# Kernel tuning notes

Measured on AMD Instinct MI355X. Metric: run time of the kernel, lower is better.

Reference implementation:

```python
import jax, jax.numpy as jnp
import numpy as np

NUM_HEADS = 16
NUM_KV_HEADS = 4
HEAD_DIM = 64
HIDDEN = 1024
B, S = 2, 2048


def setup_inputs() -> dict:
    key = jax.random.key(0)
    ks = jax.random.split(key, 9)
    sc = 0.02
    return {
        "x": jax.random.normal(ks[0], (B, S, HIDDEN), dtype=jnp.float32),
        "Wq": jax.random.normal(ks[1], (HIDDEN, NUM_HEADS * HEAD_DIM), dtype=jnp.float32) * sc,
        "bq": jnp.zeros((NUM_HEADS * HEAD_DIM,), dtype=jnp.float32),
        "Wk": jax.random.normal(ks[2], (HIDDEN, NUM_KV_HEADS * HEAD_DIM), dtype=jnp.float32) * sc,
        "bk": jnp.zeros((NUM_KV_HEADS * HEAD_DIM,), dtype=jnp.float32),
        "Wv": jax.random.normal(ks[3], (HIDDEN, NUM_KV_HEADS * HEAD_DIM), dtype=jnp.float32) * sc,
        "bv": jnp.zeros((NUM_KV_HEADS * HEAD_DIM,), dtype=jnp.float32),
        "Wo": jax.random.normal(ks[4], (NUM_HEADS * HEAD_DIM, HIDDEN), dtype=jnp.float32) * sc,
        "bo": jnp.zeros((HIDDEN,), dtype=jnp.float32),
    }


def reference(x, Wq, bq, Wk, bk, Wv, bv, Wo, bo):
    bs, seq, _ = x.shape
    groups = NUM_HEADS // NUM_KV_HEADS
    # projections -> [B, H, S, D]
    q = (x @ Wq + bq).reshape(bs, seq, NUM_HEADS, HEAD_DIM).transpose(0, 2, 1, 3)
    k = (x @ Wk + bk).reshape(bs, seq, NUM_KV_HEADS, HEAD_DIM).transpose(0, 2, 1, 3)
    v = (x @ Wv + bv).reshape(bs, seq, NUM_KV_HEADS, HEAD_DIM).transpose(0, 2, 1, 3)
    # repeat_interleave KV heads to match query heads (GQA expansion)
    k = jnp.repeat(k, groups, axis=1)
    v = jnp.repeat(v, groups, axis=1)
    # NOTE: source applies NO 1/sqrt(d) scaling and no mask/ALiBi
    scores = jnp.einsum("bhqd,bhkd->bhqk", q, k)
    attn = jax.nn.softmax(scores.astype(jnp.float32), axis=-1).astype(q.dtype)
    out = jnp.einsum("bhqk,bhkd->bhqd", attn, v)
    out = out.transpose(0, 2, 1, 3).reshape(bs, seq, NUM_HEADS * HEAD_DIM)
    return out @ Wo + bo
```

## Files before the change

### kernel.cpp

```cpp
#include <hip/hip_runtime.h>

#define NHEADS 16
#define NKV    4
#define HDIM   64
#define HIDDEN 1024
#define BATCH  2
#define SEQ    2048
#define MROWS  (BATCH * SEQ)
#define LOG2E  1.44269504088896340736f

typedef __bf16 bf16_t;
typedef bf16_t bf16x8 __attribute__((ext_vector_type(8)));
typedef float  f32x4  __attribute__((ext_vector_type(4)));

__device__ __forceinline__ float bf2f(unsigned short u) {
    return __uint_as_float(((unsigned int)u) << 16);
}
__device__ __forceinline__ unsigned short f2bf(float f) {
    unsigned int u = __float_as_uint(f);
    u += 0x7FFFu + ((u >> 16) & 1u);
    return (unsigned short)(u >> 16);
}

__device__ __forceinline__ void gld16(const unsigned short* g, unsigned short* l)
{
    __builtin_amdgcn_global_load_lds(
        (const __attribute__((address_space(1))) void*)g,
        (__attribute__((address_space(3))) void*)l,
        16, 0, 0);
}

__device__ __forceinline__ int swz(int row, int ch) {
    return (row * 8 + (ch ^ (row & 7))) * 8;
}
__device__ __forceinline__ int swz16(int row, int ch) {
    return (row * 16 + (ch ^ (row & 7))) * 8;
}

__device__ __forceinline__ bool sniff_is_f32(const unsigned short* __restrict__ x)
{
    const int e = (x[threadIdx.x & 63] >> 7) & 0xFF;
    const unsigned long long ok = __ballot(e >= 110 && e <= 140);
    return __popcll(ok) < 56;
}

__device__ __forceinline__ void load8cvt(const void* base, size_t elem, bool isf32, unsigned short out[8])
{
    if (!isf32) {
        *(uint4*)out = *(const uint4*)((const unsigned short*)base + elem);
    } else {
        const float* p = (const float*)base + elem;
        float4 v0 = *(const float4*)p;
        float4 v1 = *(const float4*)(p + 4);
        out[0] = f2bf(v0.x); out[1] = f2bf(v0.y); out[2] = f2bf(v0.z); out[3] = f2bf(v0.w);
        out[4] = f2bf(v1.x); out[5] = f2bf(v1.y); out[6] = f2bf(v1.z); out[7] = f2bf(v1.w);
    }
}
__device__ __forceinline__ float bias_at(const void* b, int i, bool isf32)
{
    return isf32 ? ((const float*)b)[i] : bf2f(((const unsigned short*)b)[i]);
}

__global__ __launch_bounds__(256)
void prep_kernel(const void* __restrict__ x,
                 const void* __restrict__ Wq, const void* __restrict__ Wk,
                 const void* __restrict__ Wv, const void* __restrict__ Wo,
                 unsigned short* __restrict__ xb,
                 unsigned short* __restrict__ Wqkvt,
                 unsigned short* __restrict__ Wot)
{
    const bool isf32 = sniff_is_f32((const unsigned short*)x);
    const int t = threadIdx.x;
    int bid = blockIdx.x;

    if (bid < 2048) {
        if (!isf32) return;
        const size_t c = (size_t)bid * 256 + t;
        unsigned short v[8];
        load8cvt(x, c * 8, true, v);
        *(uint4*)(&xb[c * 8]) = *(uint4*)v;
        return;
    }
    bid -= 2048;
    const void* src; unsigned short* dst; int N, rowoff;
    if (bid < 256)      {             src = Wq; dst = Wqkvt; N = 1024; rowoff = 0;    }
    else if (bid < 320) { bid -= 256; src = Wk; dst = Wqkvt; N = 256;  rowoff = 1024; }
    else if (bid < 384) { bid -= 320; src = Wv; dst = Wqkvt; N = 256;  rowoff = 1280; }
    else                { bid -= 384; src = Wo; dst = Wot;   N = 1024; rowoff = 0;    }
    const int ntx = N / 64;
    const int gn0 = (bid % ntx) * 64;
    const int gk0 = (bid / ntx) * 64;

    __shared__ unsigned short Ts[64][72];
#pragma unroll
    for (int half = 0; half < 2; ++half) {
        const int kl = (t >> 3) + half * 32;
        const int n8 = (t & 7) * 8;
        unsigned short v[8];
        load8cvt(src, (size_t)(gk0 + kl) * N + gn0 + n8, isf32, v);
        *(uint4*)(&Ts[kl][n8]) = *(uint4*)v;
    }
    __syncthreads();
#pragma unroll
    for (int half = 0; half < 2; ++half) {
        const int nl = (t >> 3) + half * 32;
        const int k8 = (t & 7) * 8;
        unsigned short v[8];
#pragma unroll
        for (int j = 0; j < 8; ++j) v[j] = Ts[k8 + j][nl];
        *(uint4*)(&dst[(size_t)(rowoff + gn0 + nl) * HIDDEN + gk0 + k8]) = *(uint4*)v;
    }
}

template<int TBM, int TBN>
__device__ __forceinline__ void gemm_tile(const unsigned short* __restrict__ A,
                                          const unsigned short* __restrict__ Bt,
                                          int K, int m0, int n0,
                                          unsigned short* As, unsigned short* Bs,
                                          f32x4 (&acc)[TBM / 32][TBN / 32])
{
    const int tid  = threadIdx.x;
    const int lane = tid & 63;
    const int wave = tid >> 6;
    const int quad = lane >> 4;
    const int l15  = lane & 15;
    const int wr   = wave >> 1;
    const int wc   = wave & 1;

    for (int k0 = 0; k0 < K; k0 += 128) {
#pragma unroll
        for (int r = 0; r < TBM / 16; ++r) {
            const int u = r * 256 + tid;
            const int row = u >> 4;
            const int gch = ((u & 15) ^ (row & 7)) * 8;
            gld16(&A[(size_t)(m0 + row) * K + k0 + gch], &As[(r * 256 + wave * 64) * 8]);
        }
#pragma unroll
        for (int r = 0; r < TBN / 16; ++r) {
            const int u = r * 256 + tid;
            const int row = u >> 4;
            const int gch = ((u & 15) ^ (row & 7)) * 8;
            gld16(&Bt[(size_t)(n0 + row) * K + k0 + gch], &Bs[(r * 256 + wave * 64) * 8]);
        }
        __syncthreads();

#pragma unroll
        for (int kk = 0; kk < 4; ++kk) {
            bf16x8 af[TBM / 32], bfv[TBN / 32];
#pragma unroll
            for (int i = 0; i < TBM / 32; ++i)
                af[i] = *(const bf16x8*)(&As[swz16(wr * (TBM / 2) + i * 16 + l15, kk * 4 + quad)]);
#pragma unroll
            for (int j = 0; j < TBN / 32; ++j)
                bfv[j] = *(const bf16x8*)(&Bs[swz16(wc * (TBN / 2) + j * 16 + l15, kk * 4 + quad)]);
#pragma unroll
            for (int i = 0; i < TBM / 32; ++i)
#pragma unroll
                for (int j = 0; j < TBN / 32; ++j)
                    acc[i][j] = __builtin_amdgcn_mfma_f32_16x16x32_bf16(af[i], bfv[j], acc[i][j], 0, 0, 0);
        }
        __syncthreads();
    }
}

__global__ __launch_bounds__(256)
void gemm_qkv(const void* __restrict__ xraw,
              const unsigned short* __restrict__ xb,
              const unsigned short* __restrict__ Bt,
              const void* __restrict__ bq, const void* __restrict__ bk,
              const void* __restrict__ bv,
              unsigned short* __restrict__ Qh,
              unsigned short* __restrict__ Kh,
              unsigned short* __restrict__ Vt)
{
    __shared__ __align__(16) unsigned short As[128 * 128];
    __shared__ __align__(16) unsigned short Bs[64 * 128];
    const bool bias_f32 = sniff_is_f32((const unsigned short*)xraw);
    const unsigned short* A = bias_f32 ? xb : (const unsigned short*)xraw;
    const int lane = threadIdx.x & 63;
    const int wave = threadIdx.x >> 6;
    const int quad = lane >> 4, l15 = lane & 15;
    const int wr = wave >> 1, wc = wave & 1;
    const int m0 = blockIdx.y * 128, n0 = blockIdx.x * 64;

    f32x4 acc[4][2] = {};
    gemm_tile<128, 64>(A, Bt, HIDDEN, m0, n0, As, Bs, acc);

#pragma unroll
    for (int i = 0; i < 4; ++i) {
#pragma unroll
        for (int j = 0; j < 2; ++j) {
            const int nn  = n0 + wc * 32 + j * 16 + l15;
            const int mmb = m0 + wr * 64 + i * 16 + quad * 4;
            const int b = mmb >> 11, s0 = mmb & 2047;
            if (nn < 1024) {
                const float bias = bias_at(bq, nn, bias_f32);
                const int h = nn >> 6, d = nn & 63;
                const size_t idx0 = (((size_t)(b * NHEADS + h)) * SEQ + s0) * 64 + d;
#pragma unroll
                for (int r = 0; r < 4; ++r)
                    Qh[idx0 + (size_t)r * 64] = f2bf((acc[i][j][r] + bias) * LOG2E);
            } else if (nn < 1280) {
                const int nk = nn - 1024;
                const float bias = bias_at(bk, nk, bias_f32);
                const int h = nk >> 6, d = nk & 63;
                const size_t idx0 = (((size_t)(b * NKV + h)) * SEQ + s0) * 64 + d;
#pragma unroll
                for (int r = 0; r < 4; ++r)
                    Kh[idx0 + (size_t)r * 64] = f2bf(acc[i][j][r] + bias);
            } else {
                const int nv = nn - 1280;
                const float bias = bias_at(bv, nv, bias_f32);
                const int h = nv >> 6, d = nv & 63;
                const size_t idx = (((size_t)(b * NKV + h)) * 64 + d) * SEQ + s0;
                unsigned short vv[4];
#pragma unroll
                for (int r = 0; r < 4; ++r) vv[r] = f2bf(acc[i][j][r] + bias);
                *(uint2*)(&Vt[idx]) = *(uint2*)vv;
            }
        }
    }
}

__global__ __launch_bounds__(256)
void gemm_o(const void* __restrict__ xraw,
            const unsigned short* __restrict__ A,
            const unsigned short* __restrict__ Bt,
            const void* __restrict__ bo,
            float* __restrict__ out)
{
    __shared__ __align__(16) unsigned short As[128 * 128];
    __shared__ __align__(16) unsigned short Bs[64 * 128];
    const bool bias_f32 = sniff_is_f32((const unsigned short*)xraw);
    const int lane = threadIdx.x & 63;
    const int wave = threadIdx.x >> 6;
    const int quad = lane >> 4, l15 = lane & 15;
    const int wr = wave >> 1, wc = wave & 1;
    const int m0 = blockIdx.y * 128, n0 = blockIdx.x * 64;

    f32x4 acc[4][2] = {};
    gemm_tile<128, 64>(A, Bt, HIDDEN, m0, n0, As, Bs, acc);

#pragma unroll
    for (int i = 0; i < 4; ++i) {
#pragma unroll
        for (int j = 0; j < 2; ++j) {
            const int nn = n0 + wc * 32 + j * 16 + l15;
            const float bvv = bias_at(bo, nn, bias_f32);
#pragma unroll
            for (int r = 0; r < 4; ++r) {
                const int mm = m0 + wr * 64 + i * 16 + quad * 4 + r;
                out[(size_t)mm * HIDDEN + nn] = acc[i][j][r] + bvv;
            }
        }
    }
}

#define PLD 68
#define NT  (SEQ / 64)

__device__ __forceinline__ void attn_stage(const unsigned short* __restrict__ Kt,
                                           const unsigned short* __restrict__ Vtc,
                                           unsigned short* Kd, unsigned short* Vd,
                                           int tid)
{
    const int wave  = tid >> 6;
    const int srow0 = tid >> 3;
    const int schp  = tid & 7;
#pragma unroll
    for (int c = 0; c < 2; ++c) {
        const int row = srow0 + c * 32;
        const int gch = (schp ^ (row & 7)) * 8;
        gld16(&Kt[(size_t)row * HDIM + gch], &Kd[(c * 256 + wave * 64) * 8]);
        gld16(&Vtc[(size_t)row * SEQ + gch], &Vd[(c * 256 + wave * 64) * 8]);
    }
}

__global__ __launch_bounds__(256)
void attn_kernel(const unsigned short* __restrict__ Qh,
                 const unsigned short* __restrict__ Kh,
                 const unsigned short* __restrict__ Vt,
                 unsigned short* __restrict__ O)
{
    __shared__ __align__(16) unsigned short Kth[2][64 * 64];
    __shared__ __align__(16) unsigned short VtT[2][64 * 64];
    __shared__ __align__(16) unsigned short Pt[4][32 * PLD];

    const int tid  = threadIdx.x;
    const int lane = tid & 63;
    const int wave = tid >> 6;
    const int quad = lane >> 4;
    const int l15  = lane & 15;

    const int qt = blockIdx.x;
    const int h  = blockIdx.y;
    const int b  = blockIdx.z;
    const int kv = h >> 2;

    const size_t qoff = ((size_t)(b * NHEADS + h)) * SEQ * HDIM;
    const size_t koff = ((size_t)(b * NKV + kv)) * SEQ * HDIM;
    const size_t voff = ((size_t)(b * NKV + kv)) * HDIM * SEQ;

    const int q0 = qt * 128 + wave * 32;

    bf16x8 qf0[2], qf1[2];
#pragma unroll
    for (int qs = 0; qs < 2; ++qs) {
        const size_t qrow = qoff + (size_t)(q0 + qs * 16 + l15) * HDIM;
        qf0[qs] = *(const bf16x8*)(&Qh[qrow + quad * 8]);
        qf1[qs] = *(const bf16x8*)(&Qh[qrow + 32 + quad * 8]);
    }

    f32x4 o0[4] = {}, o1[4] = {};
    f32x4 ls0 = {}, ls1 = {};

    const unsigned short* Khs = Kh + koff;
    const unsigned short* Vts = Vt + voff;

    attn_stage(Khs, Vts, &Kth[0][0], &VtT[0][0], tid);

    for (int kt = 0; kt < NT; ++kt) {
        __syncthreads();
        const int cur = kt & 1;
        if (kt + 1 < NT)
            attn_stage(Khs + (size_t)(kt + 1) * 64 * HDIM,
                       Vts + (size_t)(kt + 1) * 64,
                       &Kth[cur ^ 1][0], &VtT[cur ^ 1][0], tid);

        const unsigned short* Kc = &Kth[cur][0];
        const unsigned short* Vc = &VtT[cur][0];

#pragma unroll
        for (int j = 0; j < 4; ++j) {
            const int rr = j * 16 + l15;
            const bf16x8 kh0 = *(const bf16x8*)(&Kc[swz(rr, quad)]);
            const bf16x8 kh1 = *(const bf16x8*)(&Kc[swz(rr, quad ^ 4)]);
#pragma unroll
            for (int qs = 0; qs < 2; ++qs) {
                f32x4 z = {};
                z = __builtin_amdgcn_mfma_f32_16x16x32_bf16(kh0, qs ? qf0[1] : qf0[0], z, 0, 0, 0);
                const f32x4 sc = __builtin_amdgcn_mfma_f32_16x16x32_bf16(kh1, qs ? qf1[1] : qf1[0], z, 0, 0, 0);
                const float p0 = __builtin_amdgcn_exp2f(sc[0]);
                const float p1 = __builtin_amdgcn_exp2f(sc[1]);
                const float p2 = __builtin_amdgcn_exp2f(sc[2]);
                const float p3 = __builtin_amdgcn_exp2f(sc[3]);
                const f32x4 pv = {p0, p1, p2, p3};
                if (qs == 0) ls0 += pv; else ls1 += pv;
                uint2 w;
                w.x = __builtin_amdgcn_perm(__float_as_uint(p1), __float_as_uint(p0), 0x07060302u);
                w.y = __builtin_amdgcn_perm(__float_as_uint(p3), __float_as_uint(p2), 0x07060302u);
                *(uint2*)(&Pt[wave][(qs * 16 + l15) * PLD + j * 16 + quad * 4]) = w;
            }
        }

#pragma unroll
        for (int kk = 0; kk < 2; ++kk) {
            const bf16x8 pf0 = *(const bf16x8*)(&Pt[wave][l15 * PLD + kk * 32 + quad * 8]);
            const bf16x8 pf1 = *(const bf16x8*)(&Pt[wave][(16 + l15) * PLD + kk * 32 + quad * 8]);
#pragma unroll
            for (int dt = 0; dt < 4; ++dt) {
                const bf16x8 vf = *(const bf16x8*)(&Vc[swz(dt * 16 + l15, kk * 4 + quad)]);
                o0[dt] = __builtin_amdgcn_mfma_f32_16x16x32_bf16(vf, pf0, o0[dt], 0, 0, 0);
                o1[dt] = __builtin_amdgcn_mfma_f32_16x16x32_bf16(vf, pf1, o1[dt], 0, 0, 0);
            }
        }
    }

#pragma unroll
    for (int qs = 0; qs < 2; ++qs) {
        const f32x4 lv = qs ? ls1 : ls0;
        float lsum = (lv[0] + lv[1]) + (lv[2] + lv[3]);
        lsum += __shfl_xor(lsum, 16);
        lsum += __shfl_xor(lsum, 32);
        const float inv = 1.0f / lsum;
        const size_t rowbase = ((size_t)b * SEQ + (q0 + qs * 16 + l15)) * (NHEADS * HDIM) + h * HDIM;
#pragma unroll
        for (int dt = 0; dt < 4; ++dt) {
            const f32x4 ov = qs ? o1[dt] : o0[dt];
            unsigned short v4[4];
#pragma unroll
            for (int r = 0; r < 4; ++r) v4[r] = f2bf(ov[r] * inv);
            *(uint2*)(&O[rowbase + dt * 16 + quad * 4]) = *(uint2*)v4;
        }
    }
}

extern "C" void kernel_launch(void* const* d_in, const int* in_sizes, int n_in,
                              void* d_out, int out_size, void* d_ws, size_t ws_size,
                              hipStream_t stream)
{
    const void* x  = d_in[0];
    const void* Wq = d_in[1];
    const void* bq = d_in[2];
    const void* Wk = d_in[3];
    const void* bk = d_in[4];
    const void* Wv = d_in[5];
    const void* bv = d_in[6];
    const void* Wo = d_in[7];
    const void* bo = d_in[8];
    float* out = (float*)d_out;

    unsigned short* p = (unsigned short*)d_ws;
    unsigned short* xb    = p; p += (size_t)MROWS * HIDDEN;
    unsigned short* Wqkvt = p; p += (size_t)1536 * HIDDEN;
    unsigned short* Wot   = p; p += (size_t)HIDDEN * HIDDEN;
    unsigned short* Qh = p;  p += (size_t)MROWS * 1024;
    unsigned short* Kh = p;  p += (size_t)2 * NKV * SEQ * HDIM;
    unsigned short* Vt = p;  p += (size_t)2 * NKV * SEQ * HDIM;
    unsigned short* A2 = p;  p += (size_t)MROWS * 1024;

    dim3 blk(256);
    prep_kernel<<<dim3(2688), blk, 0, stream>>>(x, Wq, Wk, Wv, Wo, xb, Wqkvt, Wot);
    gemm_qkv<<<dim3(1536 / 64, MROWS / 128), blk, 0, stream>>>(
        x, xb, Wqkvt, bq, bk, bv, Qh, Kh, Vt);
    attn_kernel<<<dim3(SEQ / 128, NHEADS, BATCH), blk, 0, stream>>>(Qh, Kh, Vt, A2);
    gemm_o<<<dim3(1024 / 64, MROWS / 128), blk, 0, stream>>>(x, A2, Wot, bo, out);
}
```

Measured before the change: 185.6 us.

## Double-buffer GEMM K-tiles, compute softmax row sums via MFMA, add setprio

The projection GEMMs now use 64-wide K tiles in a double-buffered LDS ring, so the next tile's global-to-LDS loads overlap the current tile's MFMAs. This removes the trailing barrier and the load stall of the old single-buffer loop. The attention kernel precomputes its LDS offsets and moves the row-sum of exp scores onto MFMA against a ones vector, instead of VALU adds plus cross-lane shuffles. It also pads the P buffer differently and adds s_setprio around the MFMA blocks. The risks are summing bf16-rounded probabilities, which changes numerics slightly, and extra MFMA work in the attention loop.

```diff
diff --git a/kernel.cpp b/kernel.cpp
--- a/kernel.cpp
+++ b/kernel.cpp
@@ -32,9 +32,6 @@
 
 __device__ __forceinline__ int swz(int row, int ch) {
     return (row * 8 + (ch ^ (row & 7))) * 8;
-}
-__device__ __forceinline__ int swz16(int row, int ch) {
-    return (row * 16 + (ch ^ (row & 7))) * 8;
 }
 
 __device__ __forceinline__ bool sniff_is_f32(const unsigned short* __restrict__ x)
@@ -112,10 +109,10 @@
     }
 }
 
-template<int TBM, int TBN>
+template<int TBM, int TBN, int KK>
 __device__ __forceinline__ void gemm_tile(const unsigned short* __restrict__ A,
                                           const unsigned short* __restrict__ Bt,
-                                          int K, int m0, int n0,
+                                          int m0, int n0,
                                           unsigned short* As, unsigned short* Bs,
                                           f32x4 (&acc)[TBM / 32][TBN / 32])
 {
@@ -127,40 +124,72 @@
     const int wr   = wave >> 1;
     const int wc   = wave & 1;
 
-    for (int k0 = 0; k0 < K; k0 += 128) {
-#pragma unroll
-        for (int r = 0; r < TBM / 16; ++r) {
-            const int u = r * 256 + tid;
-            const int row = u >> 4;
-            const int gch = ((u & 15) ^ (row & 7)) * 8;
-            gld16(&A[(size_t)(m0 + row) * K + k0 + gch], &As[(r * 256 + wave * 64) * 8]);
-        }
-#pragma unroll
-        for (int r = 0; r < TBN / 16; ++r) {
-            const int u = r * 256 + tid;
-            const int row = u >> 4;
-            const int gch = ((u & 15) ^ (row & 7)) * 8;
-            gld16(&Bt[(size_t)(n0 + row) * K + k0 + gch], &Bs[(r * 256 + wave * 64) * 8]);
-        }
+    const int srow = tid >> 3;
+    const int gch  = ((tid & 7) ^ (srow & 7)) * 8;
+
+    const unsigned short* ga[TBM / 32];
+    const unsigned short* gb[TBN / 32];
+#pragma unroll
+    for (int r = 0; r < TBM / 32; ++r)
+        ga[r] = A + (size_t)(m0 + srow + r * 32) * KK + gch;
+#pragma unroll
+    for (int r = 0; r < TBN / 32; ++r)
+        gb[r] = Bt + (size_t)(n0 + srow + r * 32) * KK + gch;
+
+    const int ldw = wave * 512;
+
+    int aoffs[2][TBM / 32], boffs[2][TBN / 32];
+#pragma unroll
+    for (int kk = 0; kk < 2; ++kk) {
+#pragma unroll
+        for (int i = 0; i < TBM / 32; ++i)
+            aoffs[kk][i] = swz(wr * (TBM / 2) + i * 16 + l15, kk * 4 + quad);
+#pragma unroll
+        for (int j = 0; j < TBN / 32; ++j)
+            boffs[kk][j] = swz(wc * (TBN / 2) + j * 16 + l15, kk * 4 + quad);
+    }
+
+#define GEMM_STAGE(buf)                                                         \
+    do {                                                                        \
+        _Pragma("unroll")                                                       \
+        for (int r = 0; r < TBM / 32; ++r) {                                    \
+            gld16(ga[r], &As[(buf) * TBM * 64 + r * 2048 + ldw]);               \
+            ga[r] += 64;                                                        \
+        }                                                                       \
+        _Pragma("unroll")                                                       \
+        for (int r = 0; r < TBN / 32; ++r) {                                    \
+            gld16(gb[r], &Bs[(buf) * TBN * 64 + r * 2048 + ldw]);               \
+            gb[r] += 64;                                                        \
+        }                                                                       \
+    } while (0)
+
+    constexpr int nk = KK / 64;
+    GEMM_STAGE(0);
+#pragma unroll
+    for (int k = 0; k < nk; ++k) {
+        const int cur = k & 1;
         __syncthreads();
-
-#pragma unroll
-        for (int kk = 0; kk < 4; ++kk) {
+        if (k + 1 < nk) GEMM_STAGE(cur ^ 1);
+
+#pragma unroll
+        for (int kk = 0; kk < 2; ++kk) {
             bf16x8 af[TBM / 32], bfv[TBN / 32];
 #pragma unroll
             for (int i = 0; i < TBM / 32; ++i)
-                af[i] = *(const bf16x8*)(&As[swz16(wr * (TBM / 2) + i * 16 + l15, kk * 4 + quad)]);
+                af[i] = *(const bf16x8*)(&As[cur * TBM * 64 + aoffs[kk][i]]);
 #pragma unroll
             for (int j = 0; j < TBN / 32; ++j)
-                bfv[j] = *(const bf16x8*)(&Bs[swz16(wc * (TBN / 2) + j * 16 + l15, kk * 4 + quad)]);
+                bfv[j] = *(const bf16x8*)(&Bs[cur * TBN * 64 + boffs[kk][j]]);
+            __builtin_amdgcn_s_setprio(1);
 #pragma unroll
             for (int i = 0; i < TBM / 32; ++i)
 #pragma unroll
                 for (int j = 0; j < TBN / 32; ++j)
                     acc[i][j] = __builtin_amdgcn_mfma_f32_16x16x32_bf16(af[i], bfv[j], acc[i][j], 0, 0, 0);
-        }
-        __syncthreads();
-    }
+            __builtin_amdgcn_s_setprio(0);
+        }
+    }
+#undef GEMM_STAGE
 }
 
 __global__ __launch_bounds__(256)
@@ -173,8 +202,8 @@
               unsigned short* __restrict__ Kh,
               unsigned short* __restrict__ Vt)
 {
-    __shared__ __align__(16) unsigned short As[128 * 128];
-    __shared__ __align__(16) unsigned short Bs[64 * 128];
+    __shared__ __align__(16) unsigned short As[2 * 128 * 64];
+    __shared__ __align__(16) unsigned short Bs[2 * 64 * 64];
     const bool bias_f32 = sniff_is_f32((const unsigned short*)xraw);
     const unsigned short* A = bias_f32 ? xb : (const unsigned short*)xraw;
     const int lane = threadIdx.x & 63;
@@ -184,7 +213,7 @@
     const int m0 = blockIdx.y * 128, n0 = blockIdx.x * 64;
 
     f32x4 acc[4][2] = {};
-    gemm_tile<128, 64>(A, Bt, HIDDEN, m0, n0, As, Bs, acc);
+    gemm_tile<128, 64, HIDDEN>(A, Bt, m0, n0, As, Bs, acc);
 
 #pragma unroll
     for (int i = 0; i < 4; ++i) {
@@ -229,8 +258,8 @@
             const void* __restrict__ bo,
             float* __restrict__ out)
 {
-    __shared__ __align__(16) unsigned short As[128 * 128];
-    __shared__ __align__(16) unsigned short Bs[64 * 128];
+    __shared__ __align__(16) unsigned short As[2 * 128 * 64];
+    __shared__ __align__(16) unsigned short Bs[2 * 64 * 64];
     const bool bias_f32 = sniff_is_f32((const unsigned short*)xraw);
     const int lane = threadIdx.x & 63;
     const int wave = threadIdx.x >> 6;
@@ -239,7 +268,7 @@
     const int m0 = blockIdx.y * 128, n0 = blockIdx.x * 64;
 
     f32x4 acc[4][2] = {};
-    gemm_tile<128, 64>(A, Bt, HIDDEN, m0, n0, As, Bs, acc);
+    gemm_tile<128, 64, HIDDEN>(A, Bt, m0, n0, As, Bs, acc);
 
 #pragma unroll
     for (int i = 0; i < 4; ++i) {
@@ -256,25 +285,9 @@
     }
 }
 
-#define PLD 68
-#define NT  (SEQ / 64)
-
-__device__ __forceinline__ void attn_stage(const unsigned short* __restrict__ Kt,
-                                           const unsigned short* __restrict__ Vtc,
-                                           unsigned short* Kd, unsigned short* Vd,
-                                           int tid)
-{
-    const int wave  = tid >> 6;
-    const int srow0 = tid >> 3;
-    const int schp  = tid & 7;
-#pragma unroll
-    for (int c = 0; c < 2; ++c) {
-        const int row = srow0 + c * 32;
-        const int gch = (schp ^ (row & 7)) * 8;
-        gld16(&Kt[(size_t)row * HDIM + gch], &Kd[(c * 256 + wave * 64) * 8]);
-        gld16(&Vtc[(size_t)row * SEQ + gch], &Vd[(c * 256 + wave * 64) * 8]);
-    }
-}
+#define PLD   72
+#define NT    (SEQ / 64)
+#define KVOFF (64 * 64)
 
 __global__ __launch_bounds__(256)
 void attn_kernel(const unsigned short* __restrict__ Qh,
@@ -282,9 +295,9 @@
                  const unsigned short* __restrict__ Vt,
                  unsigned short* __restrict__ O)
 {
-    __shared__ __align__(16) unsigned short Kth[2][64 * 64];
-    __shared__ __align__(16) unsigned short VtT[2][64 * 64];
-    __shared__ __align__(16) unsigned short Pt[4][32 * PLD];
+    __shared__ __align__(16) unsigned short Kth[2 * KVOFF];
+    __shared__ __align__(16) unsigned short VtT[2 * KVOFF];
+    __shared__ __align__(16) unsigned short Pt[4 * 32 * PLD];
 
     const int tid  = threadIdx.x;
     const int lane = tid & 63;
@@ -311,68 +324,94 @@
         qf1[qs] = *(const bf16x8*)(&Qh[qrow + 32 + quad * 8]);
     }
 
+    bf16x8 onesv;
+#pragma unroll
+    for (int i = 0; i < 8; ++i) onesv[i] = (bf16_t)1.0f;
+
     f32x4 o0[4] = {}, o1[4] = {};
-    f32x4 ls0 = {}, ls1 = {};
-
-    const unsigned short* Khs = Kh + koff;
-    const unsigned short* Vts = Vt + voff;
-
-    attn_stage(Khs, Vts, &Kth[0][0], &VtT[0][0], tid);
-
+    f32x4 lacc0 = {}, lacc1 = {};
+
+    int koff0[4], koff1[4], pw[2][4], prd[2], voffs[2][4];
+#pragma unroll
+    for (int j = 0; j < 4; ++j) {
+        koff0[j] = swz(j * 16 + l15, quad);
+        koff1[j] = swz(j * 16 + l15, quad ^ 4);
+        pw[0][j] = wave * 32 * PLD + l15 * PLD + j * 16 + quad * 4;
+        pw[1][j] = pw[0][j] + 16 * PLD;
+    }
+#pragma unroll
+    for (int kk = 0; kk < 2; ++kk) {
+        prd[kk] = wave * 32 * PLD + l15 * PLD + kk * 32 + quad * 8;
+#pragma unroll
+        for (int dt = 0; dt < 4; ++dt)
+            voffs[kk][dt] = swz(dt * 16 + l15, kk * 4 + quad);
+    }
+
+    const unsigned short* kp = Kh + koff;
+    const unsigned short* vp = Vt + voff;
+    const int srow0 = tid >> 3;
+    const int gch_s = ((tid & 7) ^ (srow0 & 7)) * 8;
+
+#define ATTN_STAGE(buf)                                                          \
+    do {                                                                         \
+        gld16(kp + (size_t)srow0 * HDIM + gch_s,        &Kth[(buf)*KVOFF + wave * 512]);        \
+        gld16(kp + (size_t)(srow0 + 32) * HDIM + gch_s, &Kth[(buf)*KVOFF + 2048 + wave * 512]); \
+        gld16(vp + (size_t)srow0 * SEQ + gch_s,         &VtT[(buf)*KVOFF + wave * 512]);        \
+        gld16(vp + (size_t)(srow0 + 32) * SEQ + gch_s,  &VtT[(buf)*KVOFF + 2048 + wave * 512]); \
+        kp += 64 * HDIM; vp += 64;                                               \
+    } while (0)
+
+    ATTN_STAGE(0);
+
+#pragma unroll 2
     for (int kt = 0; kt < NT; ++kt) {
+        const int cur = kt & 1;
         __syncthreads();
-        const int cur = kt & 1;
-        if (kt + 1 < NT)
-            attn_stage(Khs + (size_t)(kt + 1) * 64 * HDIM,
-                       Vts + (size_t)(kt + 1) * 64,
-                       &Kth[cur ^ 1][0], &VtT[cur ^ 1][0], tid);
-
-        const unsigned short* Kc = &Kth[cur][0];
-        const unsigned short* Vc = &VtT[cur][0];
+        if (kt + 1 < NT) ATTN_STAGE(cur ^ 1);
 
 #pragma unroll
         for (int j = 0; j < 4; ++j) {
-            const int rr = j * 16 + l15;
-            const bf16x8 kh0 = *(const bf16x8*)(&Kc[swz(rr, quad)]);
-            const bf16x8 kh1 = *(const bf16x8*)(&Kc[swz(rr, quad ^ 4)]);
+            const bf16x8 kh0 = *(const bf16x8*)(&Kth[cur * KVOFF + koff0[j]]);
+            const bf16x8 kh1 = *(const bf16x8*)(&Kth[cur * KVOFF + koff1[j]]);
 #pragma unroll
             for (int qs = 0; qs < 2; ++qs) {
                 f32x4 z = {};
+                __builtin_amdgcn_s_setprio(1);
                 z = __builtin_amdgcn_mfma_f32_16x16x32_bf16(kh0, qs ? qf0[1] : qf0[0], z, 0, 0, 0);
                 const f32x4 sc = __builtin_amdgcn_mfma_f32_16x16x32_bf16(kh1, qs ? qf1[1] : qf1[0], z, 0, 0, 0);
+                __builtin_amdgcn_s_setprio(0);
                 const float p0 = __builtin_amdgcn_exp2f(sc[0]);
                 const float p1 = __builtin_amdgcn_exp2f(sc[1]);
                 const float p2 = __builtin_amdgcn_exp2f(sc[2]);
                 const float p3 = __builtin_amdgcn_exp2f(sc[3]);
-                const f32x4 pv = {p0, p1, p2, p3};
-                if (qs == 0) ls0 += pv; else ls1 += pv;
                 uint2 w;
                 w.x = __builtin_amdgcn_perm(__float_as_uint(p1), __float_as_uint(p0), 0x07060302u);
                 w.y = __builtin_amdgcn_perm(__float_as_uint(p3), __float_as_uint(p2), 0x07060302u);
-                *(uint2*)(&Pt[wave][(qs * 16 + l15) * PLD + j * 16 + quad * 4]) = w;
+                *(uint2*)(&Pt[pw[qs][j]]) = w;
             }
         }
 
 #pragma unroll
         for (int kk = 0; kk < 2; ++kk) {
-            const bf16x8 pf0 = *(const bf16x8*)(&Pt[wave][l15 * PLD + kk * 32 + quad * 8]);
-            const bf16x8 pf1 = *(const bf16x8*)(&Pt[wave][(16 + l15) * PLD + kk * 32 + quad * 8]);
+            const bf16x8 pf0 = *(const bf16x8*)(&Pt[prd[kk]]);
+            const bf16x8 pf1 = *(const bf16x8*)(&Pt[prd[kk] + 16 * PLD]);
+            __builtin_amdgcn_s_setprio(1);
+            lacc0 = __builtin_amdgcn_mfma_f32_16x16x32_bf16(onesv, pf0, lacc0, 0, 0, 0);
+            lacc1 = __builtin_amdgcn_mfma_f32_16x16x32_bf16(onesv, pf1, lacc1, 0, 0, 0);
 #pragma unroll
             for (int dt = 0; dt < 4; ++dt) {
-                const bf16x8 vf = *(const bf16x8*)(&Vc[swz(dt * 16 + l15, kk * 4 + quad)]);
+                const bf16x8 vf = *(const bf16x8*)(&VtT[cur * KVOFF + voffs[kk][dt]]);
                 o0[dt] = __builtin_amdgcn_mfma_f32_16x16x32_bf16(vf, pf0, o0[dt], 0, 0, 0);
                 o1[dt] = __builtin_amdgcn_mfma_f32_16x16x32_bf16(vf, pf1, o1[dt], 0, 0, 0);
             }
-        }
-    }
+            __builtin_amdgcn_s_setprio(0);
+        }
+    }
+#undef ATTN_STAGE
 
 #pragma unroll
     for (int qs = 0; qs < 2; ++qs) {
-        const f32x4 lv = qs ? ls1 : ls0;
-        float lsum = (lv[0] + lv[1]) + (lv[2] + lv[3]);
-        lsum += __shfl_xor(lsum, 16);
-        lsum += __shfl_xor(lsum, 32);
-        const float inv = 1.0f / lsum;
+        const float inv = 1.0f / (qs ? lacc1[0] : lacc0[0]);
         const size_t rowbase = ((size_t)b * SEQ + (q0 + qs * 16 + l15)) * (NHEADS * HDIM) + h * HDIM;
 #pragma unroll
         for (int dt = 0; dt < 4; ++dt) {
```

Result: faster. 176.5 us (-4.9%).
